# Optimization experiments

Hardware: AMD Instinct MI355X
Metric: run time of the kernel (lower is better)

## Reference

```python
import jax, jax.numpy as jnp
import numpy as np

B, T, D = 8, 2048, 1024

def _ln(x, g, b, eps=1e-5):
    mu = x.mean(-1, keepdims=True)
    var = ((x - mu) ** 2).mean(-1, keepdims=True)
    return (x - mu) * jax.lax.rsqrt(var + eps) * g + b

def setup_inputs() -> dict:
    key = jax.random.key(0)
    ks = jax.random.split(key, 8)
    s = 1.0 / np.sqrt(D)
    return {
        "x": jax.random.normal(ks[0], (B, T, D), jnp.float32),
        "Wq": jax.random.normal(ks[1], (D, D), jnp.float32) * s,
        "bq": jnp.zeros((D,), jnp.float32),
        "Wk": jax.random.normal(ks[2], (D, D), jnp.float32) * s,
        "bk": jnp.zeros((D,), jnp.float32),
        "Wv": jax.random.normal(ks[3], (D, D), jnp.float32) * s,
        "bv": jnp.zeros((D,), jnp.float32),
        "pos_bias": jax.random.normal(ks[4], (T, T), jnp.float32) * 0.1,
        "ln1_g": jnp.ones((D,), jnp.float32),
        "ln1_b": jnp.zeros((D,), jnp.float32),
        "W1": jax.random.normal(ks[5], (D, 4 * D), jnp.float32) * s,
        "b1": jnp.zeros((4 * D,), jnp.float32),
        "W2": jax.random.normal(ks[6], (4 * D, D), jnp.float32) * (1.0 / np.sqrt(4 * D)),
        "b2": jnp.zeros((D,), jnp.float32),
        "ln2_g": jnp.ones((D,), jnp.float32),
        "ln2_b": jnp.zeros((D,), jnp.float32),
    }

def reference(x, Wq, bq, Wk, bk, Wv, bv, pos_bias, ln1_g, ln1_b,
              W1, b1, W2, b2, ln2_g, ln2_b):
    # --- pre-norm AFT-full attention + residual ---
    h = _ln(x, ln1_g, ln1_b)
    q = h @ Wq + bq                      # [B,T,D]
    k = h @ Wk + bk
    v = h @ Wv + bv
    # global-max stabilization (cancels in the ratio)
    ek = jnp.exp(k - jax.lax.stop_gradient(k.max()))
    ew = jnp.exp(pos_bias - jax.lax.stop_gradient(pos_bias.max()))  # [T,T]
    num = jnp.einsum('ts,bsd->btd', ew, ek * v)
    den = jnp.einsum('ts,bsd->btd', ew, ek)
    attn = jax.nn.sigmoid(q) * (num / den)
    x = attn + x
    # --- pre-norm MLP + residual ---
    h = _ln(x, ln2_g, ln2_b)
    h = jax.nn.relu(h @ W1 + b1) @ W2 + b2
    return h + x
```

## Files before the change

kernel.cpp:

```cpp
#include <hip/hip_runtime.h>
#include <hip/hip_bf16.h>
#include <stdint.h>

typedef __hip_bfloat16 bf16;
typedef __attribute__((ext_vector_type(4))) float f32x4;
typedef __attribute__((ext_vector_type(8))) short bf16x8;

#define BB   8
#define TT   2048
#define DD   1024
#define MM   (BB * TT)

enum { EPI_Q = 0, EPI_K, EPI_V, EPI_ND, EPI_MLP1, EPI_MLP2 };

static __device__ __forceinline__ void async_ld16(const bf16* g, bf16* l) {
  __builtin_amdgcn_global_load_lds(
      (const __attribute__((address_space(1))) void*)g,
      (__attribute__((address_space(3))) void*)l, 16, 0, 0);
}

template<int EPI>
__global__ __launch_bounds__(512, 2)
void gemm_bt(const bf16* __restrict__ A, const bf16* __restrict__ B,
             int M, int N, int K,
             long long strideAz, long long strideBz,
             float* __restrict__ Cf,
             bf16* __restrict__ Cb, long long strideCz,
             const float* __restrict__ bias,
             const float* __restrict__ add,
             bf16* __restrict__ ekv)
{
  (void)M;
  __shared__ __align__(16) bf16 lds[65536];

  const int tid  = threadIdx.x;
  const int wave = tid >> 6;
  const int lane = tid & 63;

  const int nwg = (int)gridDim.x;
  const int bid = (int)blockIdx.x;
  const int swz = (bid & 7) * (nwg >> 3) + (bid >> 3);
  int bn, bm, bz;
  if constexpr (EPI == EPI_ND) {
    bn = swz & 7; bm = (swz >> 3) & 7; bz = swz >> 6;
  } else {
    const int nbn = N >> 8;
    const int lnb = 31 - __clz(nbn);
    bn = swz & (nbn - 1); bm = swz >> lnb; bz = 0;
  }
  A += (size_t)bz * strideAz;
  B += (size_t)bz * strideBz;

  const int wm = (wave >> 2) * 128;
  const int wn = (wave & 3) * 64;

  const int lr = lane >> 2;
  const int lc = (((lane & 3) ^ ((lane >> 3) & 3))) * 8;
  const bf16* Ag0 = A + ((size_t)bm * 256 + wave * 32 + lr) * K + lc;
  const bf16* Bg0 = B + ((size_t)bn * 256 + wave * 32 + lr) * K + lc;
  const size_t K16 = (size_t)16 * K;
  const int ldsAW = wave * 1024;
  const int ldsBW = 32768 + wave * 1024;
  const int NT = K >> 5;

  auto stageA = [&](int tt) {
    const int bo = (tt & 3) * 8192;
    const bf16* g = Ag0 + (size_t)(tt & (NT - 1)) * 32;
    async_ld16(g,       &lds[bo + ldsAW]);
    async_ld16(g + K16, &lds[bo + ldsAW + 512]);
  };
  auto stageB = [&](int tt) {
    const int bo = (tt & 3) * 8192;
    const bf16* g = Bg0 + (size_t)(tt & (NT - 1)) * 32;
    async_ld16(g,       &lds[bo + ldsBW]);
    async_ld16(g + K16, &lds[bo + ldsBW + 512]);
  };

  f32x4 acc[8][4];
#pragma unroll
  for (int i = 0; i < 8; ++i)
#pragma unroll
    for (int j = 0; j < 4; ++j) acc[i][j] = {0.f, 0.f, 0.f, 0.f};

  stageA(0); stageB(0);
  stageA(1); stageB(1);
  stageA(2); stageB(2);
  __builtin_amdgcn_sched_barrier(0);
  asm volatile("s_waitcnt vmcnt(8)" ::: "memory");
  __builtin_amdgcn_s_barrier();
  __builtin_amdgcn_sched_barrier(0);

  const int fm32 = (lane & 15) * 32;
  const int qs = (((lane >> 4) ^ ((lane >> 1) & 3))) * 8;

  for (int t = 0; t < NT; ++t) {
    const int ab = (t & 3) * 8192 + wm * 32 + fm32 + qs;
    const int bb = 32768 + (t & 3) * 8192 + wn * 32 + fm32 + qs;
    const int tw = t + 3;

    bf16x8 bfr[4], af[4];
#pragma unroll
    for (int j = 0; j < 4; ++j) bfr[j] = *(const bf16x8*)&lds[bb + j * 512];
#pragma unroll
    for (int i = 0; i < 4; ++i) af[i] = *(const bf16x8*)&lds[ab + i * 512];
    stageA(tw);
    __builtin_amdgcn_sched_barrier(0);
    asm volatile("s_waitcnt lgkmcnt(0)" ::: "memory");
    __builtin_amdgcn_s_barrier();
    __builtin_amdgcn_sched_barrier(0);
    __builtin_amdgcn_s_setprio(1);
#pragma unroll
    for (int i = 0; i < 4; ++i)
#pragma unroll
      for (int j = 0; j < 4; ++j)
        acc[i][j] = __builtin_amdgcn_mfma_f32_16x16x32_bf16(
            af[i], bfr[j], acc[i][j], 0, 0, 0);
    __builtin_amdgcn_s_setprio(0);

#pragma unroll
    for (int i = 0; i < 4; ++i)
      af[i] = *(const bf16x8*)&lds[ab + 2048 + i * 512];
    stageB(tw);
    __builtin_amdgcn_sched_barrier(0);
    asm volatile("s_waitcnt vmcnt(8) lgkmcnt(0)" ::: "memory");
    __builtin_amdgcn_s_barrier();
    __builtin_amdgcn_sched_barrier(0);
    __builtin_amdgcn_s_setprio(1);
#pragma unroll
    for (int i = 0; i < 4; ++i)
#pragma unroll
      for (int j = 0; j < 4; ++j)
        acc[4 + i][j] = __builtin_amdgcn_mfma_f32_16x16x32_bf16(
            af[i], bfr[j], acc[4 + i][j], 0, 0, 0);
    __builtin_amdgcn_s_setprio(0);
  }

  const int cr = (lane >> 4) * 4;
  const int cc = lane & 15;
#pragma unroll
  for (int i = 0; i < 8; ++i) {
#pragma unroll
    for (int j = 0; j < 4; ++j) {
#pragma unroll
      for (int r = 0; r < 4; ++r) {
        const int gm = bm * 256 + wm + i * 16 + cr + r;
        const int gn = bn * 256 + wn + j * 16 + cc;
        float v = acc[i][j][r];
        if constexpr (EPI == EPI_Q) {
          v += bias[gn];
          Cb[(size_t)gm * N + gn] = __float2bfloat16(v);
        } else if constexpr (EPI == EPI_K) {
          v = __expf(v + bias[gm]);
          const int b = gn >> 11, t = gn & (TT - 1);
          ekv[((size_t)b << 22) + (size_t)(1024 + gm) * TT + t] =
              __float2bfloat16(v);
        } else if constexpr (EPI == EPI_V) {
          v += bias[gm];
          const int b = gn >> 11, t = gn & (TT - 1);
          const size_t base = ((size_t)b << 22);
          const float ek =
              __bfloat162float(ekv[base + (size_t)(1024 + gm) * TT + t]);
          ekv[base + (size_t)gm * TT + t] = __float2bfloat16(v * ek);
        } else if constexpr (EPI == EPI_ND) {
          Cb[(size_t)bz * strideCz + (size_t)gm * N + gn] =
              __float2bfloat16(v);
        } else if constexpr (EPI == EPI_MLP1) {
          v = fmaxf(v + bias[gn], 0.0f);
          Cb[(size_t)gm * N + gn] = __float2bfloat16(v);
        } else {
          v += bias[gn] + add[(size_t)gm * N + gn];
          Cf[(size_t)gm * N + gn] = v;
        }
      }
    }
  }
}

__global__ __launch_bounds__(256)
void transpose_cast(const float* __restrict__ W, bf16* __restrict__ Wt,
                    int K, int N)
{
  __shared__ float tile[32][33];
  const int n0 = blockIdx.x * 32, k0 = blockIdx.y * 32;
  const int tx = threadIdx.x, ty = threadIdx.y;
#pragma unroll
  for (int i = 0; i < 32; i += 8)
    tile[ty + i][tx] = W[(size_t)(k0 + ty + i) * N + n0 + tx];
  __syncthreads();
#pragma unroll
  for (int i = 0; i < 32; i += 8)
    Wt[(size_t)(n0 + ty + i) * K + k0 + tx] =
        __float2bfloat16(tile[tx][ty + i]);
}

__global__ __launch_bounds__(256)
void ew_kernel(const float* __restrict__ pb, bf16* __restrict__ ew)
{
  const size_t gid = (size_t)blockIdx.x * 256 + threadIdx.x;
  const float4 v = *(const float4*)(pb + gid * 4);
  union { bf16 h[4]; unsigned long long u; } pk;
  pk.h[0] = __float2bfloat16(__expf(v.x));
  pk.h[1] = __float2bfloat16(__expf(v.y));
  pk.h[2] = __float2bfloat16(__expf(v.z));
  pk.h[3] = __float2bfloat16(__expf(v.w));
  *(unsigned long long*)(ew + gid * 4) = pk.u;
}

__global__ __launch_bounds__(256)
void ln_kernel(const float* __restrict__ x, const float* __restrict__ g,
               const float* __restrict__ b, bf16* __restrict__ out)
{
  const int row = blockIdx.x;
  const int tid = threadIdx.x;
  const float4 v = ((const float4*)(x + (size_t)row * DD))[tid];
  float s  = v.x + v.y + v.z + v.w;
  float s2 = v.x * v.x + v.y * v.y + v.z * v.z + v.w * v.w;
#pragma unroll
  for (int o = 32; o; o >>= 1) {
    s  += __shfl_down(s, o);
    s2 += __shfl_down(s2, o);
  }
  __shared__ float red[8];
  if ((tid & 63) == 0) { red[tid >> 6] = s; red[4 + (tid >> 6)] = s2; }
  __syncthreads();
  const float ts  = red[0] + red[1] + red[2] + red[3];
  const float ts2 = red[4] + red[5] + red[6] + red[7];
  const float mu = ts * (1.0f / DD);
  const float rs = rsqrtf(ts2 * (1.0f / DD) - mu * mu + 1e-5f);
  const float4 gv = ((const float4*)g)[tid];
  const float4 bv = ((const float4*)b)[tid];
  union { bf16 h[4]; unsigned long long u; } pk;
  pk.h[0] = __float2bfloat16((v.x - mu) * rs * gv.x + bv.x);
  pk.h[1] = __float2bfloat16((v.y - mu) * rs * gv.y + bv.y);
  pk.h[2] = __float2bfloat16((v.z - mu) * rs * gv.z + bv.z);
  pk.h[3] = __float2bfloat16((v.w - mu) * rs * gv.w + bv.w);
  ((unsigned long long*)(out + (size_t)row * DD))[tid] = pk.u;
}

__global__ __launch_bounds__(256)
void combine_ln_kernel(const bf16* __restrict__ q, const bf16* __restrict__ nd,
                       const float* __restrict__ x,
                       const float* __restrict__ g, const float* __restrict__ b,
                       float* __restrict__ x2, bf16* __restrict__ hout)
{
  const int row = blockIdx.x;
  const int tid = threadIdx.x;
  const int c = tid * 4;
  const bf16* ndr = nd + (size_t)row * 2048;
  union { unsigned long long u; bf16 h[4]; } un, ud, uq;
  un.u = *(const unsigned long long*)(ndr + c);
  ud.u = *(const unsigned long long*)(ndr + 1024 + c);
  uq.u = *(const unsigned long long*)(q + (size_t)row * DD + c);
  const float4 xv = *(const float4*)(x + (size_t)row * DD + c);
  float4 o;
  o.x = xv.x + (__bfloat162float(un.h[0]) / __bfloat162float(ud.h[0])) /
                   (1.0f + __expf(-__bfloat162float(uq.h[0])));
  o.y = xv.y + (__bfloat162float(un.h[1]) / __bfloat162float(ud.h[1])) /
                   (1.0f + __expf(-__bfloat162float(uq.h[1])));
  o.z = xv.z + (__bfloat162float(un.h[2]) / __bfloat162float(ud.h[2])) /
                   (1.0f + __expf(-__bfloat162float(uq.h[2])));
  o.w = xv.w + (__bfloat162float(un.h[3]) / __bfloat162float(ud.h[3])) /
                   (1.0f + __expf(-__bfloat162float(uq.h[3])));
  *(float4*)(x2 + (size_t)row * DD + c) = o;

  float s  = o.x + o.y + o.z + o.w;
  float s2 = o.x * o.x + o.y * o.y + o.z * o.z + o.w * o.w;
#pragma unroll
  for (int off = 32; off; off >>= 1) {
    s  += __shfl_down(s, off);
    s2 += __shfl_down(s2, off);
  }
  __shared__ float red[8];
  if ((tid & 63) == 0) { red[tid >> 6] = s; red[4 + (tid >> 6)] = s2; }
  __syncthreads();
  const float ts  = red[0] + red[1] + red[2] + red[3];
  const float ts2 = red[4] + red[5] + red[6] + red[7];
  const float mu = ts * (1.0f / DD);
  const float rs = rsqrtf(ts2 * (1.0f / DD) - mu * mu + 1e-5f);
  const float4 gv = ((const float4*)g)[tid];
  const float4 bv = ((const float4*)b)[tid];
  union { bf16 h[4]; unsigned long long u; } pk;
  pk.h[0] = __float2bfloat16((o.x - mu) * rs * gv.x + bv.x);
  pk.h[1] = __float2bfloat16((o.y - mu) * rs * gv.y + bv.y);
  pk.h[2] = __float2bfloat16((o.z - mu) * rs * gv.z + bv.z);
  pk.h[3] = __float2bfloat16((o.w - mu) * rs * gv.w + bv.w);
  ((unsigned long long*)(hout + (size_t)row * DD))[tid] = pk.u;
}

extern "C" void kernel_launch(void* const* d_in, const int* in_sizes, int n_in,
                              void* d_out, int out_size, void* d_ws,
                              size_t ws_size, hipStream_t stream)
{
  (void)in_sizes; (void)n_in; (void)out_size; (void)ws_size;
  const float* x   = (const float*)d_in[0];
  const float* Wq  = (const float*)d_in[1];
  const float* bq  = (const float*)d_in[2];
  const float* Wk  = (const float*)d_in[3];
  const float* bk  = (const float*)d_in[4];
  const float* Wv  = (const float*)d_in[5];
  const float* bv  = (const float*)d_in[6];
  const float* pb  = (const float*)d_in[7];
  const float* g1  = (const float*)d_in[8];
  const float* be1 = (const float*)d_in[9];
  const float* W1  = (const float*)d_in[10];
  const float* bm1 = (const float*)d_in[11];
  const float* W2  = (const float*)d_in[12];
  const float* bm2 = (const float*)d_in[13];
  const float* g2  = (const float*)d_in[14];
  const float* be2 = (const float*)d_in[15];
  float* out = (float*)d_out;

  const size_t MiB = 1024 * 1024;
  char* w = (char*)d_ws;
  bf16* hbf = (bf16*)w;  w += (size_t)MM * DD * 2;
  bf16* wqt = (bf16*)w;  w += (size_t)DD * DD * 2;
  bf16* wkt = (bf16*)w;  w += (size_t)DD * DD * 2;
  bf16* wvt = (bf16*)w;  w += (size_t)DD * DD * 2;
  bf16* w1t = (bf16*)w;  w += (size_t)4096 * DD * 2;
  bf16* w2t = (bf16*)w;  w += (size_t)DD * 4096 * 2;
  char* scr = w;
  bf16* qbf = (bf16*)scr;
  bf16* ewb = (bf16*)(scr + 32 * MiB);
  bf16* ekv = (bf16*)(scr + 40 * MiB);
  bf16* nd  = (bf16*)(scr + 104 * MiB);
  bf16* mid = (bf16*)scr;
  float* x2 = out;

  const dim3 tb(32, 8);
  transpose_cast<<<dim3(DD / 32, DD / 32), tb, 0, stream>>>(Wq, wqt, DD, DD);
  transpose_cast<<<dim3(DD / 32, DD / 32), tb, 0, stream>>>(Wk, wkt, DD, DD);
  transpose_cast<<<dim3(DD / 32, DD / 32), tb, 0, stream>>>(Wv, wvt, DD, DD);
  transpose_cast<<<dim3(4096 / 32, DD / 32), tb, 0, stream>>>(W1, w1t, DD, 4096);
  transpose_cast<<<dim3(DD / 32, 4096 / 32), tb, 0, stream>>>(W2, w2t, 4096, DD);

  ew_kernel<<<(TT * TT / 4) / 256, 256, 0, stream>>>(pb, ewb);
  ln_kernel<<<MM, 256, 0, stream>>>(x, g1, be1, hbf);

  gemm_bt<EPI_Q><<<(MM / 256) * (DD / 256), 512, 0, stream>>>(
      hbf, wqt, MM, DD, DD, 0, 0, nullptr, qbf, 0, bq, nullptr, nullptr);
  gemm_bt<EPI_K><<<(DD / 256) * (MM / 256), 512, 0, stream>>>(
      wkt, hbf, DD, MM, DD, 0, 0, nullptr, nullptr, 0, bk, nullptr, ekv);
  gemm_bt<EPI_V><<<(DD / 256) * (MM / 256), 512, 0, stream>>>(
      wvt, hbf, DD, MM, DD, 0, 0, nullptr, nullptr, 0, bv, nullptr, ekv);
  gemm_bt<EPI_ND><<<BB * (TT / 256) * (TT / 256), 512, 0, stream>>>(
      ewb, ekv, TT, TT, TT, 0, (long long)TT * TT, nullptr, nd,
      (long long)TT * TT, nullptr, nullptr, nullptr);

  combine_ln_kernel<<<MM, 256, 0, stream>>>(qbf, nd, x, g2, be2, x2, hbf);

  gemm_bt<EPI_MLP1><<<(MM / 256) * (4096 / 256), 512, 0, stream>>>(
      hbf, w1t, MM, 4096, DD, 0, 0, nullptr, mid, 0, bm1, nullptr, nullptr);
  gemm_bt<EPI_MLP2><<<(MM / 256) * (DD / 256), 512, 0, stream>>>(
      mid, w2t, MM, DD, 4096, 0, 0, out, nullptr, 0, bm2, x2, nullptr);
}
```

Baseline: 751.7 us.

## Software-pipeline LDS fragment loads across K-tiles with double-buffered registers

Restructures the GEMM main loop so LDS fragment reads for the next K-tile are issued before the current tile's MFMAs complete. B and A fragments are held in ping-pong registers across a two-step unrolled loop. Waits are relaxed to partial lgkmcnt/vmcnt counts, so MFMAs can overlap in-flight LDS reads. This raises register pressure and relies on carefully chosen wait counts for correctness, and it still reads the tile at t+1 past the last iteration.

```diff
diff --git a/kernel.cpp b/kernel.cpp
--- a/kernel.cpp
+++ b/kernel.cpp
@@ -93,47 +93,69 @@
   const int fm32 = (lane & 15) * 32;
   const int qs = (((lane >> 4) ^ ((lane >> 1) & 3))) * 8;
 
-  for (int t = 0; t < NT; ++t) {
-    const int ab = (t & 3) * 8192 + wm * 32 + fm32 + qs;
-    const int bb = 32768 + (t & 3) * 8192 + wn * 32 + fm32 + qs;
-    const int tw = t + 3;
-
-    bf16x8 bfr[4], af[4];
-#pragma unroll
-    for (int j = 0; j < 4; ++j) bfr[j] = *(const bf16x8*)&lds[bb + j * 512];
-#pragma unroll
-    for (int i = 0; i < 4; ++i) af[i] = *(const bf16x8*)&lds[ab + i * 512];
-    stageA(tw);
-    __builtin_amdgcn_sched_barrier(0);
-    asm volatile("s_waitcnt lgkmcnt(0)" ::: "memory");
-    __builtin_amdgcn_s_barrier();
-    __builtin_amdgcn_sched_barrier(0);
-    __builtin_amdgcn_s_setprio(1);
-#pragma unroll
-    for (int i = 0; i < 4; ++i)
-#pragma unroll
-      for (int j = 0; j < 4; ++j)
-        acc[i][j] = __builtin_amdgcn_mfma_f32_16x16x32_bf16(
-            af[i], bfr[j], acc[i][j], 0, 0, 0);
-    __builtin_amdgcn_s_setprio(0);
-
-#pragma unroll
-    for (int i = 0; i < 4; ++i)
-      af[i] = *(const bf16x8*)&lds[ab + 2048 + i * 512];
-    stageB(tw);
-    __builtin_amdgcn_sched_barrier(0);
-    asm volatile("s_waitcnt vmcnt(8) lgkmcnt(0)" ::: "memory");
-    __builtin_amdgcn_s_barrier();
-    __builtin_amdgcn_sched_barrier(0);
-    __builtin_amdgcn_s_setprio(1);
-#pragma unroll
-    for (int i = 0; i < 4; ++i)
-#pragma unroll
-      for (int j = 0; j < 4; ++j)
-        acc[4 + i][j] = __builtin_amdgcn_mfma_f32_16x16x32_bf16(
-            af[i], bfr[j], acc[4 + i][j], 0, 0, 0);
-    __builtin_amdgcn_s_setprio(0);
-  }
+  bf16x8 bfrP[4], bfrN[4], afA[4], afB[4];
+
+  {
+    const int ab0 = wm * 32 + fm32 + qs;
+    const int bb0 = 32768 + wn * 32 + fm32 + qs;
+#pragma unroll
+    for (int j = 0; j < 4; ++j) bfrP[j] = *(const bf16x8*)&lds[bb0 + j * 512];
+#pragma unroll
+    for (int i = 0; i < 4; ++i) afA[i] = *(const bf16x8*)&lds[ab0 + i * 512];
+  }
+  __builtin_amdgcn_sched_barrier(0);
+
+#define TILE_BODY(t, bfrC, bfrX)                                               \
+  {                                                                            \
+    const int ab  = ((t) & 3) * 8192 + wm * 32 + fm32 + qs;                    \
+    const int abn = (((t) + 1) & 3) * 8192 + wm * 32 + fm32 + qs;              \
+    const int bbn = 32768 + (((t) + 1) & 3) * 8192 + wn * 32 + fm32 + qs;      \
+                                                        \
+    _Pragma("unroll")                                                          \
+    for (int i = 0; i < 4; ++i)                                                \
+      afB[i] = *(const bf16x8*)&lds[ab + 2048 + i * 512];                      \
+    stageA((t) + 3);                                                           \
+    __builtin_amdgcn_sched_barrier(0);                                         \
+    asm volatile("s_waitcnt vmcnt(6) lgkmcnt(4)" ::: "memory");                \
+    __builtin_amdgcn_sched_barrier(0);                                         \
+    __builtin_amdgcn_s_setprio(1);                                             \
+    _Pragma("unroll")                                                          \
+    for (int i = 0; i < 4; ++i)                                                \
+      _Pragma("unroll")                                                        \
+      for (int j = 0; j < 4; ++j)                                              \
+        acc[i][j] = __builtin_amdgcn_mfma_f32_16x16x32_bf16(                   \
+            afA[i], bfrC[j], acc[i][j], 0, 0, 0);                              \
+    __builtin_amdgcn_s_setprio(0);                                             \
+    __builtin_amdgcn_s_barrier();                                              \
+    __builtin_amdgcn_sched_barrier(0);                                         \
+                                                        \
+    _Pragma("unroll")                                                          \
+    for (int j = 0; j < 4; ++j)                                                \
+      bfrX[j] = *(const bf16x8*)&lds[bbn + j * 512];                           \
+    _Pragma("unroll")                                                          \
+    for (int i = 0; i < 4; ++i)                                                \
+      afA[i] = *(const bf16x8*)&lds[abn + i * 512];                            \
+    stageB((t) + 3);                                                           \
+    __builtin_amdgcn_sched_barrier(0);                                         \
+    asm volatile("s_waitcnt lgkmcnt(8)" ::: "memory");                         \
+    __builtin_amdgcn_sched_barrier(0);                                         \
+    __builtin_amdgcn_s_setprio(1);                                             \
+    _Pragma("unroll")                                                          \
+    for (int i = 0; i < 4; ++i)                                                \
+      _Pragma("unroll")                                                        \
+      for (int j = 0; j < 4; ++j)                                              \
+        acc[4 + i][j] = __builtin_amdgcn_mfma_f32_16x16x32_bf16(               \
+            afB[i], bfrC[j], acc[4 + i][j], 0, 0, 0);                          \
+    __builtin_amdgcn_s_setprio(0);                                             \
+    __builtin_amdgcn_s_barrier();                                              \
+    __builtin_amdgcn_sched_barrier(0);                                         \
+  }
+
+  for (int tp = 0; tp < NT; tp += 2) {
+    TILE_BODY(tp,     bfrP, bfrN);
+    TILE_BODY(tp + 1, bfrN, bfrP);
+  }
+#undef TILE_BODY
 
   const int cr = (lane >> 4) * 4;
   const int cc = lane & 15;
```

Result: faster. 732.0 us (-2.6%).
